# Kernel tuning notes

Hardware: AMD Instinct MI355X
Metric: run time of the kernel (lower is better)

## Reference

```python
import jax, jax.numpy as jnp
import numpy as np

B, C, H, W, P = 4, 256, 128, 128, 2048
THR = 0.8
EPS = 1e-5  # torch BatchNorm default eps


def setup_inputs() -> dict:
    key = jax.random.key(0)
    ks = jax.random.split(key, 4)
    return {
        "x": jax.random.normal(ks[0], (B, C, H, W), jnp.float32),
        "edge": jax.random.uniform(ks[1], (B, 1, H, W), jnp.float32),
        "conv_adj_w": jax.random.normal(ks[2], (P, P), jnp.float32) * 0.02,
        "bn_adj_gamma": jnp.ones((P,), jnp.float32),
        "bn_adj_beta": jnp.zeros((P,), jnp.float32),
        "conv_wg_w": jax.random.normal(ks[3], (C, C), jnp.float32) * 0.05,
        "bn_wg_gamma": jnp.ones((C,), jnp.float32),
        "bn_wg_beta": jnp.zeros((C,), jnp.float32),
    }


def _bn_eval(z, gamma, beta, axis):
    # inference-mode BatchNorm1d with running_mean=0, running_var=1
    shape = [1] * z.ndim
    shape[axis] = -1
    inv = 1.0 / jnp.sqrt(jnp.asarray(1.0 + EPS, z.dtype))
    return z * inv * gamma.reshape(shape) + beta.reshape(shape)


def reference(x, edge, conv_adj_w, bn_adj_gamma, bn_adj_beta,
              conv_wg_w, bn_wg_gamma, bn_wg_beta):
    b, c, h, w = x.shape
    # edge[edge < thr] = 0, then topk over flattened H*W (get_upcog)
    e = jnp.where(edge < THR, jnp.zeros((), edge.dtype), edge).reshape(b, h * w)
    _, idx = jax.lax.top_k(e, P)                      # [B, P] int32

    # ps(): gather sampled features at topk locations -> [B, P, C]
    x_flat = x.reshape(b, c, h * w)                   # [B, C, HW]
    idx_e = jnp.broadcast_to(idx[:, None, :], (b, c, P))
    g = jnp.take_along_axis(x_flat, idx_e, axis=2).transpose(0, 2, 1)  # [B, P, C]

    # GCN: node-mixing 1x1 Conv1d + BN + ReLU + residual
    z = jnp.einsum('op,bpc->boc', conv_adj_w, g)      # [B, P, C]
    z = jax.nn.relu(_bn_eval(z, bn_adj_gamma, bn_adj_beta, axis=1)) + g
    # feature-mixing 1x1 Conv1d + BN + ReLU (on transposed [B, C, P])
    t = z.transpose(0, 2, 1)                          # [B, C, P]
    t = jnp.einsum('dc,bcp->bdp', conv_wg_w, t)       # [B, C, P]
    t = jax.nn.relu(_bn_eval(t, bn_wg_gamma, bn_wg_beta, axis=1))
    reasoned = t                                      # GCN transpose + ARE permute cancel -> [B, C, P]

    # scatter reasoned features back into x (topk indices are unique)
    out = jax.vmap(lambda xf, i, r: xf.at[:, i].set(r))(x_flat, idx, reasoned)
    return out.reshape(b, c, h, w)
```

## Files before the change

### kernel.cpp

```cpp
#include <hip/hip_runtime.h>
#include <stdint.h>

#define B_   4
#define C_   256
#define HW_  16384
#define P_   2048
#define THR_ 0.8f
#define INV_ 0.9999950000374997f

#define OFF_NCAND 0
#define OFF_CAND  256
#define OFF_TOPK  524544
#define OFF_POS   557312
#define OFF_G     819456
#define OFF_GT    9208064
#define OFF_Z2    13402368
#define OFF_WADJB 17596672
#define OFF_WGB   25985280
#define OFF_R     OFF_G
#define OFF_RANK  OFF_Z2

typedef __attribute__((ext_vector_type(8))) short bf16x8;
typedef __attribute__((ext_vector_type(4))) float f32x4;

__device__ __forceinline__ ushort f2bf(float f) {
    union { float f; unsigned u; } a; a.f = f;
    unsigned r = (a.u + 0x7fffu + ((a.u >> 16) & 1u)) >> 16;
    return (ushort)r;
}

__global__ __launch_bounds__(256) void zero_ws_kernel(int* __restrict__ pos,
                                                      int* __restrict__ rankbuf,
                                                      int* __restrict__ ncand) {
    int i = blockIdx.x * 256 + threadIdx.x;
    if (i < B_ * HW_) { pos[i] = 0; rankbuf[i] = 0; }
    if (i < B_) ncand[i] = 0;
}

__global__ __launch_bounds__(256) void convert_bf16_kernel(const float* __restrict__ src,
                                                           ushort* __restrict__ dst) {
    int i = blockIdx.x * 256 + threadIdx.x;
    float4 v = ((const float4*)src)[i];
    ushort4 o; o.x = f2bf(v.x); o.y = f2bf(v.y); o.z = f2bf(v.z); o.w = f2bf(v.w);
    ((ushort4*)dst)[i] = o;
}

__global__ __launch_bounds__(256) void compact_kernel(const float* __restrict__ edge,
                                                      unsigned long long* __restrict__ cand,
                                                      int* __restrict__ ncand) {
    int b = blockIdx.x >> 6;
    int i = (blockIdx.x & 63) * 256 + threadIdx.x;
    float e = edge[b * HW_ + i];
    if (e >= THR_) {
        int slot = atomicAdd(&ncand[b], 1);
        unsigned int vb = __float_as_uint(e);
        cand[(size_t)b * HW_ + slot] =
            ((unsigned long long)vb << 32) | (unsigned long long)(0xFFFFFFFFu - (unsigned)i);
    }
}

__global__ __launch_bounds__(256) void rank_partial_kernel(
        const unsigned long long* __restrict__ cand,
        const int* __restrict__ ncand,
        int* __restrict__ rankbuf) {
    int b = blockIdx.z;
    int n = ncand[b];
    int jb = blockIdx.x * 256, tb = blockIdx.y * 256;
    if (jb >= n || tb >= n) return;
    const unsigned long long* cb = cand + (size_t)b * HW_;
    __shared__ unsigned long long tile[256];
    int j = jb + threadIdx.x;
    unsigned long long kj = (j < n) ? cb[j] : 0ull;
    tile[threadIdx.x] = (tb + (int)threadIdx.x < n) ? cb[tb + threadIdx.x] : 0ull;
    __syncthreads();
    int cnt = 0;
#pragma unroll 16
    for (int k = 0; k < 256; ++k) cnt += (tile[k] > kj) ? 1 : 0;
    if (j < n && cnt) atomicAdd(&rankbuf[b * HW_ + j], cnt);
}

__global__ __launch_bounds__(256) void rank_finalize_kernel(
        const unsigned long long* __restrict__ cand,
        const int* __restrict__ ncand,
        const int* __restrict__ rankbuf,
        int* __restrict__ topk,
        int* __restrict__ pos) {
    int b = blockIdx.y;
    int n = ncand[b];
    int j = blockIdx.x * 256 + threadIdx.x;
    if (j >= n) return;
    int rank = rankbuf[b * HW_ + j];
    if (rank < P_) {
        int idx = (int)(0xFFFFFFFFu - (unsigned)(cand[(size_t)b * HW_ + j] & 0xFFFFFFFFull));
        topk[b * P_ + rank] = idx;
        pos[b * HW_ + idx] = rank + 1;
    }
}

__global__ void fallback_kernel(const float* __restrict__ edge,
                                const int* __restrict__ ncand,
                                int* __restrict__ topk,
                                int* __restrict__ pos) {
    int b = blockIdx.x;
    int n = ncand[b];
    if (n >= P_) return;
    if (threadIdx.x != 0) return;
    int cnt = n;
    for (int i = 0; i < HW_ && cnt < P_; ++i) {
        if (edge[b * HW_ + i] < THR_) {
            topk[b * P_ + cnt] = i;
            pos[b * HW_ + i] = cnt + 1;
            cnt++;
        }
    }
}

__global__ __launch_bounds__(256) void scan_gather_kernel(const float* __restrict__ x,
                                                          const int* __restrict__ pos,
                                                          float* __restrict__ g,
                                                          ushort* __restrict__ gT) {
    size_t v = (size_t)blockIdx.x * 256 + threadIdx.x;
    size_t e0 = v * 4;
    int hw = (int)(e0 & (HW_ - 1));
    int bc = (int)(e0 >> 14);
    int c = bc & (C_ - 1);
    int b = bc >> 8;
    float4 xv = *(const float4*)&x[e0];
    int4 pv = *(const int4*)&pos[b * HW_ + hw];
    float* gb = g + (size_t)b * P_ * C_;
    ushort* gTb = gT + ((size_t)b * C_ + c) * P_;
    if (pv.x) { gb[(size_t)(pv.x - 1) * C_ + c] = xv.x; gTb[pv.x - 1] = f2bf(xv.x); }
    if (pv.y) { gb[(size_t)(pv.y - 1) * C_ + c] = xv.y; gTb[pv.y - 1] = f2bf(xv.y); }
    if (pv.z) { gb[(size_t)(pv.z - 1) * C_ + c] = xv.z; gTb[pv.z - 1] = f2bf(xv.z); }
    if (pv.w) { gb[(size_t)(pv.w - 1) * C_ + c] = xv.w; gTb[pv.w - 1] = f2bf(xv.w); }
}

#define MFMA16(AB, BB)                                                              \
    _Pragma("unroll")                                                               \
    for (int i = 0; i < 4; ++i)                                                     \
    _Pragma("unroll")                                                               \
        for (int j = 0; j < 4; ++j)                                                 \
            acc[i][j] = __builtin_amdgcn_mfma_f32_16x16x32_bf16(                    \
                __builtin_bit_cast(bf16x8, AB[i]),                                  \
                __builtin_bit_cast(bf16x8, BB[j]), acc[i][j], 0, 0, 0);

template<int MODE, int KDIM, int NTN>
__global__ __launch_bounds__(64) void gemm_wave_kernel(
        const ushort* __restrict__ A, const ushort* __restrict__ B,
        const float* __restrict__ gamma, const float* __restrict__ beta,
        const float* __restrict__ resid, void* __restrict__ out) {
    constexpr int KSTEPS = KDIM / 32;
    const int bid = blockIdx.x;
    const int mt = bid / NTN;
    const int nt = bid % NTN;
    const int lane = threadIdx.x;
    const int quad = lane >> 4, ln = lane & 15;

    const ushort* pa[4];
    const ushort* pb[4];
#pragma unroll
    for (int i = 0; i < 4; ++i) {
        pa[i] = A + (size_t)(mt * 64 + i * 16 + ln) * KDIM + quad * 8;
        pb[i] = B + (size_t)(nt * 64 + i * 16 + ln) * KDIM + quad * 8;
    }

    f32x4 acc[4][4];
#pragma unroll
    for (int i = 0; i < 4; ++i)
#pragma unroll
        for (int j = 0; j < 4; ++j) acc[i][j] = (f32x4){0.f, 0.f, 0.f, 0.f};

    uint4 a0[4], b0[4], a1[4], b1[4];
#pragma unroll
    for (int i = 0; i < 4; ++i) {
        a0[i] = *(const uint4*)(pa[i]);
        b0[i] = *(const uint4*)(pb[i]);
        a1[i] = *(const uint4*)(pa[i] + 32);
        b1[i] = *(const uint4*)(pb[i] + 32);
    }

    int koff = 64;
    for (int s = 0; s < KSTEPS - 2; s += 2) {
        MFMA16(a0, b0)
#pragma unroll
        for (int i = 0; i < 4; ++i) {
            a0[i] = *(const uint4*)(pa[i] + koff);
            b0[i] = *(const uint4*)(pb[i] + koff);
        }
        MFMA16(a1, b1)
#pragma unroll
        for (int i = 0; i < 4; ++i) {
            a1[i] = *(const uint4*)(pa[i] + koff + 32);
            b1[i] = *(const uint4*)(pb[i] + koff + 32);
        }
        koff += 64;
    }
    MFMA16(a0, b0)
    MFMA16(a1, b1)

    float gm[16], bt[16];
#pragma unroll
    for (int i = 0; i < 4; ++i)
#pragma unroll
        for (int rg = 0; rg < 4; ++rg) {
            int row = mt * 64 + i * 16 + quad * 4 + rg;
            gm[i * 4 + rg] = gamma[row] * INV_;
            bt[i * 4 + rg] = beta[row];
        }

    if (MODE == 1) {
#pragma unroll
        for (int j = 0; j < 4; ++j) {
            int n = nt * 64 + j * 16 + ln;
            int bb = n >> 8;
            int cc = n & (C_ - 1);
            const float* res = resid + (size_t)bb * P_ * C_ + cc;
            ushort* op = (ushort*)out + (size_t)bb * P_ * C_ + cc;
#pragma unroll
            for (int i = 0; i < 4; ++i)
#pragma unroll
                for (int rg = 0; rg < 4; ++rg) {
                    int row = mt * 64 + i * 16 + quad * 4 + rg;
                    float v = fmaxf(acc[i][j][rg] * gm[i * 4 + rg] + bt[i * 4 + rg], 0.f)
                              + res[(size_t)row * C_];
                    op[(size_t)row * C_] = f2bf(v);
                }
        }
    } else {
#pragma unroll
        for (int j = 0; j < 4; ++j) {
            int n = nt * 64 + j * 16 + ln;
            int bb = n >> 11;
            int pp = n & (P_ - 1);
            float* op = (float*)out + (size_t)bb * C_ * P_ + pp;
#pragma unroll
            for (int i = 0; i < 4; ++i)
#pragma unroll
                for (int rg = 0; rg < 4; ++rg) {
                    int row = mt * 64 + i * 16 + quad * 4 + rg;
                    op[(size_t)row * P_] =
                        fmaxf(acc[i][j][rg] * gm[i * 4 + rg] + bt[i * 4 + rg], 0.f);
                }
        }
    }
}

__global__ __launch_bounds__(256) void output_kernel(const float* __restrict__ x,
                                                     const int* __restrict__ pos,
                                                     const float* __restrict__ r,
                                                     float* __restrict__ out) {
    size_t v = (size_t)blockIdx.x * 256 + threadIdx.x;
    size_t e0 = v * 4;
    int hw = (int)(e0 & (HW_ - 1));
    int bc = (int)(e0 >> 14);
    int d = bc & (C_ - 1);
    int b = bc >> 8;
    float4 xv = *(const float4*)&x[e0];
    int4 pv = *(const int4*)&pos[b * HW_ + hw];
    const float* rrow = r + ((size_t)b * C_ + d) * P_;
    float4 ov = xv;
    if (pv.x) ov.x = rrow[pv.x - 1];
    if (pv.y) ov.y = rrow[pv.y - 1];
    if (pv.z) ov.z = rrow[pv.z - 1];
    if (pv.w) ov.w = rrow[pv.w - 1];
    *(float4*)&out[e0] = ov;
}

extern "C" void kernel_launch(void* const* d_in, const int* in_sizes, int n_in,
                              void* d_out, int out_size, void* d_ws, size_t ws_size,
                              hipStream_t stream) {
    const float* x    = (const float*)d_in[0];
    const float* edge = (const float*)d_in[1];
    const float* Wadj = (const float*)d_in[2];
    const float* ga   = (const float*)d_in[3];
    const float* be   = (const float*)d_in[4];
    const float* Wg   = (const float*)d_in[5];
    const float* gw   = (const float*)d_in[6];
    const float* bw   = (const float*)d_in[7];
    float* out = (float*)d_out;

    char* ws = (char*)d_ws;
    int*                ncand = (int*)(ws + OFF_NCAND);
    unsigned long long* cand  = (unsigned long long*)(ws + OFF_CAND);
    int*                topk  = (int*)(ws + OFF_TOPK);
    int*                pos   = (int*)(ws + OFF_POS);
    int*                rankb = (int*)(ws + OFF_RANK);
    float*              g     = (float*)(ws + OFF_G);
    ushort*             gT    = (ushort*)(ws + OFF_GT);
    ushort*             z2    = (ushort*)(ws + OFF_Z2);
    ushort*             WadjB = (ushort*)(ws + OFF_WADJB);
    ushort*             WgB   = (ushort*)(ws + OFF_WGB);
    float*              rbuf  = (float*)(ws + OFF_R);

    convert_bf16_kernel<<<P_ * P_ / 4 / 256, 256, 0, stream>>>(Wadj, WadjB);
    convert_bf16_kernel<<<C_ * C_ / 4 / 256, 256, 0, stream>>>(Wg, WgB);
    zero_ws_kernel<<<(B_ * HW_ + 255) / 256, 256, 0, stream>>>(pos, rankb, ncand);
    compact_kernel<<<B_ * 64, 256, 0, stream>>>(edge, cand, ncand);
    {
        dim3 grid(64, 64, B_);
        rank_partial_kernel<<<grid, 256, 0, stream>>>(cand, ncand, rankb);
    }
    {
        dim3 grid(64, B_);
        rank_finalize_kernel<<<grid, 256, 0, stream>>>(cand, ncand, rankb, topk, pos);
    }
    fallback_kernel<<<B_, 64, 0, stream>>>(edge, ncand, topk, pos);
    scan_gather_kernel<<<(B_ * C_ * HW_) / 4 / 256, 256, 0, stream>>>(x, pos, g, gT);

    gemm_wave_kernel<1, 2048, 16><<<512, 64, 0, stream>>>(WadjB, gT, ga, be, g, z2);
    gemm_wave_kernel<2, 256, 128><<<512, 64, 0, stream>>>(WgB, z2, gw, bw, nullptr, rbuf);

    output_kernel<<<(B_ * C_ * HW_) / 4 / 256, 256, 0, stream>>>(x, pos, rbuf, out);
}
```

Before: 265.5 us.

## Gather via LDS-staged rows using topk indices and drop fp32 residual copy

Replaces the scatter-style gather, which wrote both an fp32 [B,P,C] copy and a bf16 transposed copy with strided scattered stores, with a per-(b,c) block. Each block stages one x row in LDS and gathers the 2048 topk entries into the bf16 transposed buffer with coalesced vector stores. The first GEMM's residual now reads the bf16 transposed buffer instead of the fp32 copy, which removes one buffer write and the strided fp32 residual reads. The trade-off is that the residual is now rounded to bf16, which costs some accuracy, and each block holds a 64KB LDS allocation that limits occupancy.

```diff
diff --git a/kernel.cpp b/kernel.cpp
--- a/kernel.cpp
+++ b/kernel.cpp
@@ -27,6 +27,10 @@
     union { float f; unsigned u; } a; a.f = f;
     unsigned r = (a.u + 0x7fffu + ((a.u >> 16) & 1u)) >> 16;
     return (ushort)r;
+}
+__device__ __forceinline__ float bf2f(ushort u) {
+    union { unsigned u; float f; } a; a.u = (unsigned)u << 16;
+    return a.f;
 }
 
 __global__ __launch_bounds__(256) void zero_ws_kernel(int* __restrict__ pos,
@@ -115,24 +119,27 @@
     }
 }
 
-__global__ __launch_bounds__(256) void scan_gather_kernel(const float* __restrict__ x,
-                                                          const int* __restrict__ pos,
-                                                          float* __restrict__ g,
-                                                          ushort* __restrict__ gT) {
-    size_t v = (size_t)blockIdx.x * 256 + threadIdx.x;
-    size_t e0 = v * 4;
-    int hw = (int)(e0 & (HW_ - 1));
-    int bc = (int)(e0 >> 14);
-    int c = bc & (C_ - 1);
+__global__ __launch_bounds__(256) void gather_lds_kernel(const float* __restrict__ x,
+                                                         const int* __restrict__ topk,
+                                                         ushort* __restrict__ gT) {
+    __shared__ float row[HW_];
+    int bc = blockIdx.x;
     int b = bc >> 8;
-    float4 xv = *(const float4*)&x[e0];
-    int4 pv = *(const int4*)&pos[b * HW_ + hw];
-    float* gb = g + (size_t)b * P_ * C_;
-    ushort* gTb = gT + ((size_t)b * C_ + c) * P_;
-    if (pv.x) { gb[(size_t)(pv.x - 1) * C_ + c] = xv.x; gTb[pv.x - 1] = f2bf(xv.x); }
-    if (pv.y) { gb[(size_t)(pv.y - 1) * C_ + c] = xv.y; gTb[pv.y - 1] = f2bf(xv.y); }
-    if (pv.z) { gb[(size_t)(pv.z - 1) * C_ + c] = xv.z; gTb[pv.z - 1] = f2bf(xv.z); }
-    if (pv.w) { gb[(size_t)(pv.w - 1) * C_ + c] = xv.w; gTb[pv.w - 1] = f2bf(xv.w); }
+    const float* xr = x + (size_t)bc * HW_;
+#pragma unroll
+    for (int i = 0; i < 16; ++i)
+        ((float4*)row)[threadIdx.x + i * 256] = ((const float4*)xr)[threadIdx.x + i * 256];
+    __syncthreads();
+    const int* tk = topk + b * P_;
+    int p0 = threadIdx.x * 8;
+    int4 i0 = *(const int4*)&tk[p0];
+    int4 i1 = *(const int4*)&tk[p0 + 4];
+    ushort4 o0, o1;
+    o0.x = f2bf(row[i0.x]); o0.y = f2bf(row[i0.y]); o0.z = f2bf(row[i0.z]); o0.w = f2bf(row[i0.w]);
+    o1.x = f2bf(row[i1.x]); o1.y = f2bf(row[i1.y]); o1.z = f2bf(row[i1.z]); o1.w = f2bf(row[i1.w]);
+    ushort* gp = gT + (size_t)bc * P_ + p0;
+    *(ushort4*)gp = o0;
+    *(ushort4*)(gp + 4) = o1;
 }
 
 #define MFMA16(AB, BB)                                                              \
@@ -148,7 +155,7 @@
 __global__ __launch_bounds__(64) void gemm_wave_kernel(
         const ushort* __restrict__ A, const ushort* __restrict__ B,
         const float* __restrict__ gamma, const float* __restrict__ beta,
-        const float* __restrict__ resid, void* __restrict__ out) {
+        const ushort* __restrict__ residT, void* __restrict__ out) {
     constexpr int KSTEPS = KDIM / 32;
     const int bid = blockIdx.x;
     const int mt = bid / NTN;
@@ -214,17 +221,20 @@
             int n = nt * 64 + j * 16 + ln;
             int bb = n >> 8;
             int cc = n & (C_ - 1);
-            const float* res = resid + (size_t)bb * P_ * C_ + cc;
+            const ushort* gr = residT + (size_t)n * P_;
             ushort* op = (ushort*)out + (size_t)bb * P_ * C_ + cc;
 #pragma unroll
-            for (int i = 0; i < 4; ++i)
+            for (int i = 0; i < 4; ++i) {
+                int rbase = mt * 64 + i * 16 + quad * 4;
+                ushort4 rv = *(const ushort4*)&gr[rbase];
+                float rf[4] = {bf2f(rv.x), bf2f(rv.y), bf2f(rv.z), bf2f(rv.w)};
 #pragma unroll
                 for (int rg = 0; rg < 4; ++rg) {
-                    int row = mt * 64 + i * 16 + quad * 4 + rg;
-                    float v = fmaxf(acc[i][j][rg] * gm[i * 4 + rg] + bt[i * 4 + rg], 0.f)
-                              + res[(size_t)row * C_];
+                    int row = rbase + rg;
+                    float v = fmaxf(acc[i][j][rg] * gm[i * 4 + rg] + bt[i * 4 + rg], 0.f) + rf[rg];
                     op[(size_t)row * C_] = f2bf(v);
                 }
+            }
         }
     } else {
 #pragma unroll
@@ -285,7 +295,6 @@
     int*                topk  = (int*)(ws + OFF_TOPK);
     int*                pos   = (int*)(ws + OFF_POS);
     int*                rankb = (int*)(ws + OFF_RANK);
-    float*              g     = (float*)(ws + OFF_G);
     ushort*             gT    = (ushort*)(ws + OFF_GT);
     ushort*             z2    = (ushort*)(ws + OFF_Z2);
     ushort*             WadjB = (ushort*)(ws + OFF_WADJB);
@@ -305,9 +314,9 @@
         rank_finalize_kernel<<<grid, 256, 0, stream>>>(cand, ncand, rankb, topk, pos);
     }
     fallback_kernel<<<B_, 64, 0, stream>>>(edge, ncand, topk, pos);
-    scan_gather_kernel<<<(B_ * C_ * HW_) / 4 / 256, 256, 0, stream>>>(x, pos, g, gT);
-
-    gemm_wave_kernel<1, 2048, 16><<<512, 64, 0, stream>>>(WadjB, gT, ga, be, g, z2);
+    gather_lds_kernel<<<B_ * C_, 256, 0, stream>>>(x, topk, gT);
+
+    gemm_wave_kernel<1, 2048, 16><<<512, 64, 0, stream>>>(WadjB, gT, ga, be, gT, z2);
     gemm_wave_kernel<2, 256, 128><<<512, 64, 0, stream>>>(WgB, z2, gw, bw, nullptr, rbuf);
 
     output_kernel<<<(B_ * C_ * HW_) / 4 / 256, 256, 0, stream>>>(x, pos, rbuf, out);
```

Measured after the change: 235.7 us. 11.2% less time.
